# Kernel optimization log

Measured on AMD Instinct MI355X. Metric: run time of the kernel, lower is better.

The kernel has to match this reference:

```python
import jax, jax.numpy as jnp
import numpy as np

N = 1 << 20          # query points
IN_DIMS = 32
HIDDEN = 64
N_INNER = 4          # n_hidden_layers - 1 hidden->hidden layers
OUT_DIMS = 3


def _kaiming(key, shape):
    fan_in = shape[-1]
    bound = np.sqrt(6.0 / fan_in)  # kaiming_uniform with relu gain sqrt(2): sqrt(6/fan_in)
    return jax.random.uniform(key, shape, jnp.float32, -bound, bound)


def setup_inputs() -> dict:
    key = jax.random.key(0)
    ks = jax.random.split(key, 4)
    x = jax.random.normal(ks[0], (N, IN_DIMS), jnp.float32)
    W_in = _kaiming(ks[1], (HIDDEN, IN_DIMS))
    b_in = jnp.zeros((HIDDEN,), jnp.float32)
    W_hid = _kaiming(ks[2], (N_INNER, HIDDEN, HIDDEN))
    b_hid = jnp.zeros((N_INNER, HIDDEN), jnp.float32)
    W_out = _kaiming(ks[3], (OUT_DIMS, HIDDEN))
    b_out = jnp.zeros((OUT_DIMS,), jnp.float32)
    return {"x": x, "W_in": W_in, "b_in": b_in, "W_hid": W_hid,
            "b_hid": b_hid, "W_out": W_out, "b_out": b_out}


def reference(x, W_in, b_in, W_hid, b_hid, W_out, b_out):
    # torch nn.Linear: y = x @ W.T + b
    h = jax.nn.relu(x @ W_in.T + b_in)                     # [N, HIDDEN]

    def step(h, wb):
        W, b = wb
        return jax.nn.relu(h @ W.T + b), None

    h, _ = jax.lax.scan(step, h, (W_hid, b_hid))           # 4 hidden layers
    out = h @ W_out.T + b_out                              # [N, OUT_DIMS]
    return jax.nn.sigmoid(out)                             # output_activation='Sigmoid'
```

## Files before the change

kernel.cpp:

```cpp
#include <hip/hip_runtime.h>
#include <hip/hip_bf16.h>


typedef __attribute__((ext_vector_type(8))) short bf16x8;
typedef __attribute__((ext_vector_type(4))) float f32x4;

#define NWFRAG 38
#define BIAS_F32 9728
#define IMG_BYTES 40256
#define IMG_U4 2516

struct F3 { float a, b, c; };

__device__ __forceinline__ unsigned cvtpk(float lo, float hi) {
    unsigned r;
    asm("v_cvt_pk_bf16_f32 %0, %1, %2" : "=v"(r) : "v"(lo), "v"(hi));
    return r;
}

__device__ __forceinline__ unsigned pkrelu(unsigned u, unsigned z) {
    unsigned r;
    asm("v_pk_max_i16 %0, %1, %2" : "=v"(r) : "v"(u), "v"(z));
    return r;
}

__device__ __forceinline__ int pinv(int s) {
    return ((s >> 5) & 1) * 32 + ((s >> 2) & 1) * 16 + ((s >> 3) & 3) * 4 + (s & 3);
}

__device__ uint4 frag_value_w(int F, int lane,
        const float* __restrict__ W_in, const float* __restrict__ W_hid,
        const float* __restrict__ W_out) {
    const int j = lane & 15, g = lane >> 4;
    uint4 r = {0u, 0u, 0u, 0u};
    if (F < 4) {
        const float* row = W_in + (F * 16 + j) * 32 + 8 * g;
        r.x = cvtpk(row[0], row[1]); r.y = cvtpk(row[2], row[3]);
        r.z = cvtpk(row[4], row[5]); r.w = cvtpk(row[6], row[7]);
    } else if (F < 36) {
        int q = F - 4, L = q >> 3, nt = (q >> 1) & 3, f = q & 1;
        const float* row = W_hid + (L * 64 + nt * 16 + j) * 64;
        int s0 = 32 * f + 8 * g;
        r.x = cvtpk(row[pinv(s0 + 0)], row[pinv(s0 + 1)]);
        r.y = cvtpk(row[pinv(s0 + 2)], row[pinv(s0 + 3)]);
        r.z = cvtpk(row[pinv(s0 + 4)], row[pinv(s0 + 5)]);
        r.w = cvtpk(row[pinv(s0 + 6)], row[pinv(s0 + 7)]);
    } else {
        int f = F - 36;
        if (j < 3) {
            const float* row = W_out + j * 64;
            int s0 = 32 * f + 8 * g;
            r.x = cvtpk(row[pinv(s0 + 0)], row[pinv(s0 + 1)]);
            r.y = cvtpk(row[pinv(s0 + 2)], row[pinv(s0 + 3)]);
            r.z = cvtpk(row[pinv(s0 + 4)], row[pinv(s0 + 5)]);
            r.w = cvtpk(row[pinv(s0 + 6)], row[pinv(s0 + 7)]);
        }
    }
    return r;
}

__device__ __forceinline__ float bias_val(int idx,
        const float* __restrict__ b_in, const float* __restrict__ b_hid,
        const float* __restrict__ b_out) {
    if (idx < 64)  return b_in[idx];
    if (idx < 320) return b_hid[idx - 64];
    return (idx - 320 < 3) ? b_out[idx - 320] : 0.f;
}

__global__ void prep_kernel(const float* __restrict__ W_in,  const float* __restrict__ b_in,
                            const float* __restrict__ W_hid, const float* __restrict__ b_hid,
                            const float* __restrict__ W_out, const float* __restrict__ b_out,
                            uint4* __restrict__ img) {
    const int F = blockIdx.x, t = threadIdx.x;
    if (F < NWFRAG) {
        img[F * 64 + t] = frag_value_w(F, t, W_in, W_hid, W_out);
    } else {
        float* fb = (float*)img + BIAS_F32;
        for (int idx = t; idx < 336; idx += 64)
            fb[idx] = bias_val(idx, b_in, b_hid, b_out);
    }
}

__device__ __forceinline__ void relu_pack(const f32x4 a[4], bf16x8 h[2], unsigned z) {
#pragma unroll
    for (int f = 0; f < 2; ++f) {
        union { bf16x8 v; unsigned u[4]; } t;
        t.u[0] = pkrelu(cvtpk(a[2 * f][0], a[2 * f][1]), z);
        t.u[1] = pkrelu(cvtpk(a[2 * f][2], a[2 * f][3]), z);
        t.u[2] = pkrelu(cvtpk(a[2 * f + 1][0], a[2 * f + 1][1]), z);
        t.u[3] = pkrelu(cvtpk(a[2 * f + 1][2], a[2 * f + 1][3]), z);
        h[f] = t.v;
    }
}

#define MFMA(a, b, c) __builtin_amdgcn_mfma_f32_16x16x32_bf16((a), (b), (c), 0, 0, 0)

template<bool FAST>
__global__ __launch_bounds__(512, 4) void mlp_kernel(
        const float* __restrict__ x, const uint4* __restrict__ img,
        const float* __restrict__ gW_in,  const float* __restrict__ gb_in,
        const float* __restrict__ gW_hid, const float* __restrict__ gb_hid,
        const float* __restrict__ gW_out, const float* __restrict__ gb_out,
        float* __restrict__ out) {
    __shared__ uint4 simg[IMG_U4];
    const int tid = threadIdx.x;

    if (FAST) {
#pragma unroll
        for (int i = 0; i < 5; ++i) {
            int idx = tid + i * 512;
            if (idx < IMG_U4) simg[idx] = img[idx];
        }
    } else {
        for (int idx = tid; idx < NWFRAG * 64; idx += 512)
            simg[idx] = frag_value_w(idx >> 6, idx & 63, gW_in, gW_hid, gW_out);
        {
            float* fb = (float*)simg + BIAS_F32;
            for (int idx = tid; idx < 336; idx += 512)
                fb[idx] = bias_val(idx, gb_in, gb_hid, gb_out);
        }
    }

    const int wave = tid >> 6, lane = tid & 63;
    const int j = lane & 15, g = lane >> 4;
    const int base = (blockIdx.x * 8 + wave) * 256;

    f32x4 raw[4][2];
    {
        const float* xp = x + (size_t)(base + j) * 32 + 8 * g;
#pragma unroll
        for (int t = 0; t < 4; ++t) {
            raw[t][0] = *(const f32x4*)(xp + t * 512);
            raw[t][1] = *(const f32x4*)(xp + t * 512 + 4);
        }
    }
    __syncthreads();

    const uint4*  lp = &simg[lane];
    const float*  sb = (const float*)simg + BIAS_F32;
    const unsigned z = 0;

#pragma unroll 1
    for (int it = 0; it < 4; ++it) {
        const int p0 = base + it * 64;

        bf16x8 xf[4];
#pragma unroll
        for (int t = 0; t < 4; ++t) {
            union { bf16x8 v; unsigned u[4]; } a;
            a.u[0] = cvtpk(raw[t][0][0], raw[t][0][1]);
            a.u[1] = cvtpk(raw[t][0][2], raw[t][0][3]);
            a.u[2] = cvtpk(raw[t][1][0], raw[t][1][1]);
            a.u[3] = cvtpk(raw[t][1][2], raw[t][1][3]);
            xf[t] = a.v;
        }

        bf16x8 hfrag[4][2];
        {
            f32x4 acc[4][4];
            __builtin_amdgcn_s_setprio(1);
#pragma unroll
            for (int nt = 0; nt < 4; ++nt) {
                bf16x8 w  = *(const bf16x8*)&lp[nt * 64];
                f32x4  bz = *(const f32x4*)&sb[nt * 16 + 4 * g];
#pragma unroll
                for (int t = 0; t < 4; ++t)
                    acc[t][nt] = MFMA(w, xf[t], bz);
            }
            __builtin_amdgcn_s_setprio(0);
#pragma unroll
            for (int t = 0; t < 4; ++t) relu_pack(acc[t], hfrag[t], z);
        }

#pragma unroll
        for (int L = 0; L < 4; ++L) {
            const int wb = (4 + L * 8) * 64;
            bf16x8 w0[4], w1[4]; f32x4 bz[4];
#pragma unroll
            for (int nt = 0; nt < 4; ++nt) {
                w0[nt] = *(const bf16x8*)&lp[wb + (2 * nt) * 64];
                w1[nt] = *(const bf16x8*)&lp[wb + (2 * nt + 1) * 64];
                bz[nt] = *(const f32x4*)&sb[64 + L * 64 + nt * 16 + 4 * g];
            }
#pragma unroll
            for (int pr = 0; pr < 2; ++pr) {
                f32x4 pa[2][4];
                __builtin_amdgcn_s_setprio(1);
#pragma unroll
                for (int q = 0; q < 2; ++q)
#pragma unroll
                    for (int nt = 0; nt < 4; ++nt)
                        pa[q][nt] = MFMA(w0[nt], hfrag[2 * pr + q][0], bz[nt]);
#pragma unroll
                for (int q = 0; q < 2; ++q)
#pragma unroll
                    for (int nt = 0; nt < 4; ++nt)
                        pa[q][nt] = MFMA(w1[nt], hfrag[2 * pr + q][1], pa[q][nt]);
                __builtin_amdgcn_s_setprio(0);
#pragma unroll
                for (int q = 0; q < 2; ++q) relu_pack(pa[q], hfrag[2 * pr + q], z);
            }
        }

        bf16x8 wo0 = *(const bf16x8*)&lp[36 * 64];
        bf16x8 wo1 = *(const bf16x8*)&lp[37 * 64];
        f32x4  bo  = *(const f32x4*)&sb[320 + 4 * g];
        f32x4 zacc[4];
        __builtin_amdgcn_s_setprio(1);
#pragma unroll
        for (int t = 0; t < 4; ++t) {
            f32x4 tmp = MFMA(wo0, hfrag[t][0], bo);
            zacc[t] = MFMA(wo1, hfrag[t][1], tmp);
        }
        __builtin_amdgcn_s_setprio(0);

        {
            const int pn = (it < 3) ? p0 + 64 : p0;
            const float* xp = x + (size_t)(pn + j) * 32 + 8 * g;
#pragma unroll
            for (int t = 0; t < 4; ++t) {
                raw[t][0] = *(const f32x4*)(xp + t * 512);
                raw[t][1] = *(const f32x4*)(xp + t * 512 + 4);
            }
        }

        if (g == 0) {
            float* ob = out + (size_t)(p0 + j) * 3;
#pragma unroll
            for (int t = 0; t < 4; ++t) {
                F3 v;
                v.a = __builtin_amdgcn_rcpf(1.f + __expf(-zacc[t][0]));
                v.b = __builtin_amdgcn_rcpf(1.f + __expf(-zacc[t][1]));
                v.c = __builtin_amdgcn_rcpf(1.f + __expf(-zacc[t][2]));
                *(F3*)(ob + t * 48) = v;
            }
        }
    }
}

extern "C" void kernel_launch(void* const* d_in, const int* in_sizes, int n_in,
                              void* d_out, int out_size, void* d_ws, size_t ws_size,
                              hipStream_t stream) {
    const float* x     = (const float*)d_in[0];
    const float* W_in  = (const float*)d_in[1];
    const float* b_in  = (const float*)d_in[2];
    const float* W_hid = (const float*)d_in[3];
    const float* b_hid = (const float*)d_in[4];
    const float* W_out = (const float*)d_in[5];
    const float* b_out = (const float*)d_in[6];
    float* out = (float*)d_out;

    int n = in_sizes[0] / 32;
    int nblocks = n / 2048;

    if (ws_size >= (size_t)IMG_BYTES) {
        hipLaunchKernelGGL(prep_kernel, dim3(NWFRAG + 1), dim3(64), 0, stream,
                           W_in, b_in, W_hid, b_hid, W_out, b_out, (uint4*)d_ws);
        hipLaunchKernelGGL((mlp_kernel<true>), dim3(nblocks), dim3(512), 0, stream,
                           x, (const uint4*)d_ws,
                           W_in, b_in, W_hid, b_hid, W_out, b_out, out);
    } else {
        hipLaunchKernelGGL((mlp_kernel<false>), dim3(nblocks), dim3(512), 0, stream,
                           x, (const uint4*)d_ws,
                           W_in, b_in, W_hid, b_hid, W_out, b_out, out);
    }
}
```

Measured before the change: 46.14 us.

## Switch MLP to 32x32x16 bf16 MFMA tiles with re-permuted weight image

Replaces the 16x16x32 MFMA chain with 32x32x16 bf16 MFMAs processing 32 points per iteration (8 iterations instead of 4). The weight and bias image layout is regenerated with a new permutation so each layer's output accumulator feeds the next layer's B operand directly, and ReLU moves to fmax before conversion. This lowers MFMA instruction count and register pressure per tile, but each iteration now carries a longer dependent chain with less independent work to hide latency.

```diff
diff --git a/kernel.cpp b/kernel.cpp
--- a/kernel.cpp
+++ b/kernel.cpp
@@ -4,11 +4,12 @@
 
 typedef __attribute__((ext_vector_type(8))) short bf16x8;
 typedef __attribute__((ext_vector_type(4))) float f32x4;
-
-#define NWFRAG 38
-#define BIAS_F32 9728
-#define IMG_BYTES 40256
-#define IMG_U4 2516
+typedef __attribute__((ext_vector_type(16))) float f32x16;
+
+#define NWFRAG 40
+#define BIAS_F32 10240
+#define IMG_BYTES 42368
+#define IMG_U4 2648
 
 struct F3 { float a, b, c; };
 
@@ -18,42 +19,38 @@
     return r;
 }
 
-__device__ __forceinline__ unsigned pkrelu(unsigned u, unsigned z) {
-    unsigned r;
-    asm("v_pk_max_i16 %0, %1, %2" : "=v"(r) : "v"(u), "v"(z));
-    return r;
-}
-
-__device__ __forceinline__ int pinv(int s) {
-    return ((s >> 5) & 1) * 32 + ((s >> 2) & 1) * 16 + ((s >> 3) & 3) * 4 + (s & 3);
+__device__ __forceinline__ int pinv32(int s) {
+    return ((s >> 5) & 1) * 32 + ((s >> 4) & 1) * 16 + ((s >> 2) & 1) * 8 +
+           ((s >> 3) & 1) * 4 + ((s >> 1) & 1) * 2 + (s & 1);
 }
 
 __device__ uint4 frag_value_w(int F, int lane,
         const float* __restrict__ W_in, const float* __restrict__ W_hid,
         const float* __restrict__ W_out) {
-    const int j = lane & 15, g = lane >> 4;
+    const int j = lane & 31, hi = lane >> 5;
     uint4 r = {0u, 0u, 0u, 0u};
     if (F < 4) {
-        const float* row = W_in + (F * 16 + j) * 32 + 8 * g;
+        int nt = F >> 1, K = F & 1;
+        const float* row = W_in + (nt * 32 + j) * 32 + K * 16 + hi * 8;
         r.x = cvtpk(row[0], row[1]); r.y = cvtpk(row[2], row[3]);
         r.z = cvtpk(row[4], row[5]); r.w = cvtpk(row[6], row[7]);
     } else if (F < 36) {
-        int q = F - 4, L = q >> 3, nt = (q >> 1) & 3, f = q & 1;
-        const float* row = W_hid + (L * 64 + nt * 16 + j) * 64;
-        int s0 = 32 * f + 8 * g;
-        r.x = cvtpk(row[pinv(s0 + 0)], row[pinv(s0 + 1)]);
-        r.y = cvtpk(row[pinv(s0 + 2)], row[pinv(s0 + 3)]);
-        r.z = cvtpk(row[pinv(s0 + 4)], row[pinv(s0 + 5)]);
-        r.w = cvtpk(row[pinv(s0 + 6)], row[pinv(s0 + 7)]);
-    } else {
-        int f = F - 36;
+        int q = F - 4, L = q >> 3, nt = (q >> 2) & 1, K = q & 3;
+        const float* row = W_hid + (L * 64 + nt * 32 + j) * 64;
+        int s0 = K * 16 + hi * 8;
+        r.x = cvtpk(row[pinv32(s0 + 0)], row[pinv32(s0 + 1)]);
+        r.y = cvtpk(row[pinv32(s0 + 2)], row[pinv32(s0 + 3)]);
+        r.z = cvtpk(row[pinv32(s0 + 4)], row[pinv32(s0 + 5)]);
+        r.w = cvtpk(row[pinv32(s0 + 6)], row[pinv32(s0 + 7)]);
+    } else {
+        int K = F - 36;
         if (j < 3) {
             const float* row = W_out + j * 64;
-            int s0 = 32 * f + 8 * g;
-            r.x = cvtpk(row[pinv(s0 + 0)], row[pinv(s0 + 1)]);
-            r.y = cvtpk(row[pinv(s0 + 2)], row[pinv(s0 + 3)]);
-            r.z = cvtpk(row[pinv(s0 + 4)], row[pinv(s0 + 5)]);
-            r.w = cvtpk(row[pinv(s0 + 6)], row[pinv(s0 + 7)]);
+            int s0 = K * 16 + hi * 8;
+            r.x = cvtpk(row[pinv32(s0 + 0)], row[pinv32(s0 + 1)]);
+            r.y = cvtpk(row[pinv32(s0 + 2)], row[pinv32(s0 + 3)]);
+            r.z = cvtpk(row[pinv32(s0 + 4)], row[pinv32(s0 + 5)]);
+            r.w = cvtpk(row[pinv32(s0 + 6)], row[pinv32(s0 + 7)]);
         }
     }
     return r;
@@ -62,9 +59,16 @@
 __device__ __forceinline__ float bias_val(int idx,
         const float* __restrict__ b_in, const float* __restrict__ b_hid,
         const float* __restrict__ b_out) {
-    if (idx < 64)  return b_in[idx];
-    if (idx < 320) return b_hid[idx - 64];
-    return (idx - 320 < 3) ? b_out[idx - 320] : 0.f;
+    if (idx < 64) {
+        int nt = idx >> 5, hi = (idx >> 4) & 1, rr = idx & 15;
+        return b_in[nt * 32 + (rr & 3) + 8 * ((rr >> 2) & 3) + 4 * hi];
+    }
+    if (idx < 320) {
+        int q = idx - 64, L = q >> 6, nt = (q >> 5) & 1, hi = (q >> 4) & 1, rr = q & 15;
+        return b_hid[L * 64 + nt * 32 + (rr & 3) + 8 * ((rr >> 2) & 3) + 4 * hi];
+    }
+    int q = idx - 320, hi = q >> 4, rr = q & 15;
+    return (hi == 0 && rr < 3) ? b_out[rr] : 0.f;
 }
 
 __global__ void prep_kernel(const float* __restrict__ W_in,  const float* __restrict__ b_in,
@@ -76,24 +80,26 @@
         img[F * 64 + t] = frag_value_w(F, t, W_in, W_hid, W_out);
     } else {
         float* fb = (float*)img + BIAS_F32;
-        for (int idx = t; idx < 336; idx += 64)
+        for (int idx = t; idx < 352; idx += 64)
             fb[idx] = bias_val(idx, b_in, b_hid, b_out);
     }
 }
 
-__device__ __forceinline__ void relu_pack(const f32x4 a[4], bf16x8 h[2], unsigned z) {
-#pragma unroll
-    for (int f = 0; f < 2; ++f) {
-        union { bf16x8 v; unsigned u[4]; } t;
-        t.u[0] = pkrelu(cvtpk(a[2 * f][0], a[2 * f][1]), z);
-        t.u[1] = pkrelu(cvtpk(a[2 * f][2], a[2 * f][3]), z);
-        t.u[2] = pkrelu(cvtpk(a[2 * f + 1][0], a[2 * f + 1][1]), z);
-        t.u[3] = pkrelu(cvtpk(a[2 * f + 1][2], a[2 * f + 1][3]), z);
-        h[f] = t.v;
-    }
-}
-
-#define MFMA(a, b, c) __builtin_amdgcn_mfma_f32_16x16x32_bf16((a), (b), (c), 0, 0, 0)
+template<int C>
+__device__ __forceinline__ bf16x8 fragof(f32x16 a) {
+    union { bf16x8 v; unsigned u[4]; } t;
+    t.u[0] = cvtpk(fmaxf(a[8 * C + 0], 0.f), fmaxf(a[8 * C + 1], 0.f));
+    t.u[1] = cvtpk(fmaxf(a[8 * C + 2], 0.f), fmaxf(a[8 * C + 3], 0.f));
+    t.u[2] = cvtpk(fmaxf(a[8 * C + 4], 0.f), fmaxf(a[8 * C + 5], 0.f));
+    t.u[3] = cvtpk(fmaxf(a[8 * C + 6], 0.f), fmaxf(a[8 * C + 7], 0.f));
+    return t.v;
+}
+
+__device__ __forceinline__ f32x16 ldbias(const float* sb, int off, int hi) {
+    return *(const f32x16*)(sb + off + hi * 16);
+}
+
+#define MFMA32(a, b, c) __builtin_amdgcn_mfma_f32_32x32x16_bf16((a), (b), (c), 0, 0, 0)
 
 template<bool FAST>
 __global__ __launch_bounds__(512, 4) void mlp_kernel(
@@ -102,12 +108,12 @@
         const float* __restrict__ gW_hid, const float* __restrict__ gb_hid,
         const float* __restrict__ gW_out, const float* __restrict__ gb_out,
         float* __restrict__ out) {
-    __shared__ uint4 simg[IMG_U4];
+    __shared__ __attribute__((aligned(64))) uint4 simg[IMG_U4];
     const int tid = threadIdx.x;
 
     if (FAST) {
 #pragma unroll
-        for (int i = 0; i < 5; ++i) {
+        for (int i = 0; i < 6; ++i) {
             int idx = tid + i * 512;
             if (idx < IMG_U4) simg[idx] = img[idx];
         }
@@ -116,123 +122,91 @@
             simg[idx] = frag_value_w(idx >> 6, idx & 63, gW_in, gW_hid, gW_out);
         {
             float* fb = (float*)simg + BIAS_F32;
-            for (int idx = tid; idx < 336; idx += 512)
+            for (int idx = tid; idx < 352; idx += 512)
                 fb[idx] = bias_val(idx, gb_in, gb_hid, gb_out);
         }
     }
 
     const int wave = tid >> 6, lane = tid & 63;
-    const int j = lane & 15, g = lane >> 4;
+    const int j = lane & 31, hi = lane >> 5;
     const int base = (blockIdx.x * 8 + wave) * 256;
 
-    f32x4 raw[4][2];
+    f32x4 raw[4];
     {
-        const float* xp = x + (size_t)(base + j) * 32 + 8 * g;
-#pragma unroll
-        for (int t = 0; t < 4; ++t) {
-            raw[t][0] = *(const f32x4*)(xp + t * 512);
-            raw[t][1] = *(const f32x4*)(xp + t * 512 + 4);
-        }
+        const float* xp = x + (size_t)(base + j) * 32 + hi * 8;
+        raw[0] = *(const f32x4*)xp;        raw[1] = *(const f32x4*)(xp + 4);
+        raw[2] = *(const f32x4*)(xp + 16); raw[3] = *(const f32x4*)(xp + 20);
     }
     __syncthreads();
 
     const uint4*  lp = &simg[lane];
     const float*  sb = (const float*)simg + BIAS_F32;
-    const unsigned z = 0;
 
 #pragma unroll 1
-    for (int it = 0; it < 4; ++it) {
-        const int p0 = base + it * 64;
-
-        bf16x8 xf[4];
-#pragma unroll
-        for (int t = 0; t < 4; ++t) {
-            union { bf16x8 v; unsigned u[4]; } a;
-            a.u[0] = cvtpk(raw[t][0][0], raw[t][0][1]);
-            a.u[1] = cvtpk(raw[t][0][2], raw[t][0][3]);
-            a.u[2] = cvtpk(raw[t][1][0], raw[t][1][1]);
-            a.u[3] = cvtpk(raw[t][1][2], raw[t][1][3]);
-            xf[t] = a.v;
-        }
-
-        bf16x8 hfrag[4][2];
-        {
-            f32x4 acc[4][4];
+    for (int it = 0; it < 8; ++it) {
+        bf16x8 xf0, xf1;
+        {
+            union { bf16x8 v; unsigned u[4]; } t0, t1;
+            t0.u[0] = cvtpk(raw[0][0], raw[0][1]);
+            t0.u[1] = cvtpk(raw[0][2], raw[0][3]);
+            t0.u[2] = cvtpk(raw[1][0], raw[1][1]);
+            t0.u[3] = cvtpk(raw[1][2], raw[1][3]);
+            t1.u[0] = cvtpk(raw[2][0], raw[2][1]);
+            t1.u[1] = cvtpk(raw[2][2], raw[2][3]);
+            t1.u[2] = cvtpk(raw[3][0], raw[3][1]);
+            t1.u[3] = cvtpk(raw[3][2], raw[3][3]);
+            xf0 = t0.v; xf1 = t1.v;
+        }
+
+        {
+            const int itn = (it < 7) ? it + 1 : it;
+            const float* xp = x + (size_t)(base + itn * 32 + j) * 32 + hi * 8;
+            raw[0] = *(const f32x4*)xp;        raw[1] = *(const f32x4*)(xp + 4);
+            raw[2] = *(const f32x4*)(xp + 16); raw[3] = *(const f32x4*)(xp + 20);
+        }
+
+        bf16x8 h0, h1, h2, h3;
+        {
             __builtin_amdgcn_s_setprio(1);
-#pragma unroll
-            for (int nt = 0; nt < 4; ++nt) {
-                bf16x8 w  = *(const bf16x8*)&lp[nt * 64];
-                f32x4  bz = *(const f32x4*)&sb[nt * 16 + 4 * g];
-#pragma unroll
-                for (int t = 0; t < 4; ++t)
-                    acc[t][nt] = MFMA(w, xf[t], bz);
-            }
+            f32x16 a0 = MFMA32(*(const bf16x8*)&lp[0 * 64], xf0, ldbias(sb, 0, hi));
+            a0 = MFMA32(*(const bf16x8*)&lp[1 * 64], xf1, a0);
+            f32x16 a1 = MFMA32(*(const bf16x8*)&lp[2 * 64], xf0, ldbias(sb, 32, hi));
+            a1 = MFMA32(*(const bf16x8*)&lp[3 * 64], xf1, a1);
             __builtin_amdgcn_s_setprio(0);
-#pragma unroll
-            for (int t = 0; t < 4; ++t) relu_pack(acc[t], hfrag[t], z);
-        }
-
+            h0 = fragof<0>(a0); h1 = fragof<1>(a0);
+            h2 = fragof<0>(a1); h3 = fragof<1>(a1);
+        }
 #pragma unroll
         for (int L = 0; L < 4; ++L) {
-            const int wb = (4 + L * 8) * 64;
-            bf16x8 w0[4], w1[4]; f32x4 bz[4];
-#pragma unroll
-            for (int nt = 0; nt < 4; ++nt) {
-                w0[nt] = *(const bf16x8*)&lp[wb + (2 * nt) * 64];
-                w1[nt] = *(const bf16x8*)&lp[wb + (2 * nt + 1) * 64];
-                bz[nt] = *(const f32x4*)&sb[64 + L * 64 + nt * 16 + 4 * g];
-            }
-#pragma unroll
-            for (int pr = 0; pr < 2; ++pr) {
-                f32x4 pa[2][4];
-                __builtin_amdgcn_s_setprio(1);
-#pragma unroll
-                for (int q = 0; q < 2; ++q)
-#pragma unroll
-                    for (int nt = 0; nt < 4; ++nt)
-                        pa[q][nt] = MFMA(w0[nt], hfrag[2 * pr + q][0], bz[nt]);
-#pragma unroll
-                for (int q = 0; q < 2; ++q)
-#pragma unroll
-                    for (int nt = 0; nt < 4; ++nt)
-                        pa[q][nt] = MFMA(w1[nt], hfrag[2 * pr + q][1], pa[q][nt]);
-                __builtin_amdgcn_s_setprio(0);
-#pragma unroll
-                for (int q = 0; q < 2; ++q) relu_pack(pa[q], hfrag[2 * pr + q], z);
-            }
-        }
-
-        bf16x8 wo0 = *(const bf16x8*)&lp[36 * 64];
-        bf16x8 wo1 = *(const bf16x8*)&lp[37 * 64];
-        f32x4  bo  = *(const f32x4*)&sb[320 + 4 * g];
-        f32x4 zacc[4];
-        __builtin_amdgcn_s_setprio(1);
-#pragma unroll
-        for (int t = 0; t < 4; ++t) {
-            f32x4 tmp = MFMA(wo0, hfrag[t][0], bo);
-            zacc[t] = MFMA(wo1, hfrag[t][1], tmp);
-        }
-        __builtin_amdgcn_s_setprio(0);
-
-        {
-            const int pn = (it < 3) ? p0 + 64 : p0;
-            const float* xp = x + (size_t)(pn + j) * 32 + 8 * g;
-#pragma unroll
-            for (int t = 0; t < 4; ++t) {
-                raw[t][0] = *(const f32x4*)(xp + t * 512);
-                raw[t][1] = *(const f32x4*)(xp + t * 512 + 4);
-            }
-        }
-
-        if (g == 0) {
-            float* ob = out + (size_t)(p0 + j) * 3;
-#pragma unroll
-            for (int t = 0; t < 4; ++t) {
+            const int wb = (4 + L * 8);
+            const int bb = 64 + L * 64;
+            __builtin_amdgcn_s_setprio(1);
+            f32x16 a0 = MFMA32(*(const bf16x8*)&lp[(wb + 0) * 64], h0, ldbias(sb, bb, hi));
+            a0 = MFMA32(*(const bf16x8*)&lp[(wb + 1) * 64], h1, a0);
+            a0 = MFMA32(*(const bf16x8*)&lp[(wb + 2) * 64], h2, a0);
+            a0 = MFMA32(*(const bf16x8*)&lp[(wb + 3) * 64], h3, a0);
+            f32x16 a1 = MFMA32(*(const bf16x8*)&lp[(wb + 4) * 64], h0, ldbias(sb, bb + 32, hi));
+            a1 = MFMA32(*(const bf16x8*)&lp[(wb + 5) * 64], h1, a1);
+            a1 = MFMA32(*(const bf16x8*)&lp[(wb + 6) * 64], h2, a1);
+            a1 = MFMA32(*(const bf16x8*)&lp[(wb + 7) * 64], h3, a1);
+            __builtin_amdgcn_s_setprio(0);
+            h0 = fragof<0>(a0); h1 = fragof<1>(a0);
+            h2 = fragof<0>(a1); h3 = fragof<1>(a1);
+        }
+        {
+            __builtin_amdgcn_s_setprio(1);
+            f32x16 zf = MFMA32(*(const bf16x8*)&lp[36 * 64], h0, ldbias(sb, 320, hi));
+            zf = MFMA32(*(const bf16x8*)&lp[37 * 64], h1, zf);
+            zf = MFMA32(*(const bf16x8*)&lp[38 * 64], h2, zf);
+            zf = MFMA32(*(const bf16x8*)&lp[39 * 64], h3, zf);
+            __builtin_amdgcn_s_setprio(0);
+            if (hi == 0) {
+                const int p = base + it * 32 + j;
                 F3 v;
-                v.a = __builtin_amdgcn_rcpf(1.f + __expf(-zacc[t][0]));
-                v.b = __builtin_amdgcn_rcpf(1.f + __expf(-zacc[t][1]));
-                v.c = __builtin_amdgcn_rcpf(1.f + __expf(-zacc[t][2]));
-                *(F3*)(ob + t * 48) = v;
+                v.a = __builtin_amdgcn_rcpf(1.f + __expf(-zf[0]));
+                v.b = __builtin_amdgcn_rcpf(1.f + __expf(-zf[1]));
+                v.c = __builtin_amdgcn_rcpf(1.f + __expf(-zf[2]));
+                *(F3*)(out + (size_t)p * 3) = v;
             }
         }
     }
```

Measured after the change: 57.28 us. +24.1%, slower.
